# Kernel tuning notes

Hardware: AMD Instinct MI355X
Metric: run time of the kernel (lower is better)

Reference implementation:

```python
import jax, jax.numpy as jnp
import numpy as np

N = 100000   # number of nodes
E = 400000   # number of edges
C = 16       # n_in_channels == n_out_channels
L = 16       # node_conv2 .. node_conv17
EPS = 1e-5   # BatchNorm eps


def _bn(h, g, b):
    # training-mode BatchNorm1d over the edge/batch axis (biased variance)
    mu = h.mean(0)
    var = h.var(0)
    return (h - mu) * jax.lax.rsqrt(var + EPS) * g + b


def setup_inputs() -> dict:
    key = jax.random.key(0)
    ks = jax.random.split(key, 6)
    return {
        "edge_features": jax.random.normal(ks[0], (E, C), jnp.float32),
        "edge_index": jax.random.randint(ks[1], (2, E), 0, N),
        "angles": jax.random.normal(ks[2], (E,), jnp.float32),
        "Wn": jax.random.normal(ks[3], (L, C, 2 * C), jnp.float32) / np.sqrt(2.0 * C),
        "bn": jnp.zeros((L, C), jnp.float32),
        "gn": jnp.ones((L, C), jnp.float32),
        "btn": jnp.zeros((L, C), jnp.float32),
        "We": jax.random.normal(ks[4], (C, 2 * C), jnp.float32) / np.sqrt(2.0 * C),
        "be": jnp.zeros((C,), jnp.float32),
        "ge": jnp.ones((C,), jnp.float32),
        "bte": jnp.zeros((C,), jnp.float32),
    }


def _forward(edge_features, edge_index, Wn, bn, gn, btn, We, be, ge, bte):
    src, dst = edge_index[0], edge_index[1]

    # EdgeConvNoNodes: init node features = mean of incident edge features (both endpoints)
    idx = jnp.concatenate([src, dst])                       # [2E]
    feats = jnp.concatenate([edge_features, edge_features], axis=0)
    deg = jax.ops.segment_sum(jnp.ones((2 * E,), edge_features.dtype), idx, N)
    x = jax.ops.segment_sum(feats, idx, N) / jnp.clip(deg, 1.0)[:, None]  # [N, C]

    # in-degree for mean aggregation of the 16 NodeConv1 layers
    deg_in = jnp.clip(jax.ops.segment_sum(jnp.ones((E,), x.dtype), dst, N), 1.0)[:, None]

    def step(x, p):
        W, b, g, bt = p
        # message: Linear(cat(x_i, x_j)) -> BN -> LeakyReLU on [E, C]
        m = jnp.concatenate([x[dst], x[src]], axis=1) @ W.T + b
        m = jax.nn.leaky_relu(_bn(m, g, bt))
        # mean aggregation at target nodes
        return jax.ops.segment_sum(m, dst, N) / deg_in, None

    x, _ = jax.lax.scan(step, x, (Wn, bn, gn, btn))

    # EdgeConv2: per-edge MLP on both edge directions, BN stats shared over [2E]
    pair = jnp.concatenate(
        [jnp.concatenate([x[src], x[dst]], axis=1),
         jnp.concatenate([x[dst], x[src]], axis=1)], axis=0)  # [2E, 2C]
    e = jax.nn.leaky_relu(_bn(pair @ We.T + be, ge, bte))      # [2E, C]
    e_fwd, e_bwd = e[:E], e[E:]
    edge_out = 0.5 * (e_fwd + e_bwd)                           # symmetric edge feature
    side_loss = jnp.mean((e_fwd - e_bwd) ** 2)                 # symmetry side loss
    return edge_out, side_loss


def reference(edge_features, edge_index, angles, Wn, bn, gn, btn, We, be, ge, bte):
    # `angles` is accepted but unused, matching the original forward
    return _forward(edge_features, edge_index, Wn, bn, gn, btn, We, be, ge, bte)
```

## Files before the change

### kernel.cpp

```cpp
#include <hip/hip_runtime.h>
#include <hip/hip_fp16.h>
#include <cstdint>
#include <cstddef>

#define NN 100000
#define EE 400000
#define CC 16
#define LL 16
#define NB 16

typedef unsigned int uint;

__device__ __forceinline__ float lrelu(float v){ return v > 0.0f ? v : 0.01f*v; }

__device__ __forceinline__ float waveSum(float v){
#pragma unroll
  for (int off = 32; off >= 1; off >>= 1) v += __shfl_xor(v, off);
  return v;
}

__device__ __forceinline__ uint pack_h2(float a, float b){
  __half2 h = __floats2half2_rn(a, b);
  return *reinterpret_cast<uint*>(&h);
}
__device__ __forceinline__ float2 unpack_h2(uint v){
  __half2 h = *reinterpret_cast<__half2*>(&v);
  return __half22float2(h);
}

__device__ __forceinline__ void unpack_row(const uint* __restrict__ xh, int n, float* f){
  const uint4* p = (const uint4*)(xh + (size_t)n*8);
  uint4 r0 = p[0], r1 = p[1];
  uint w[8] = {r0.x,r0.y,r0.z,r0.w, r1.x,r1.y,r1.z,r1.w};
#pragma unroll
  for (int q=0;q<8;q++){ float2 v = unpack_h2(w[q]); f[2*q]=v.x; f[2*q+1]=v.y; }
}

__global__ __launch_bounds__(256) void k_count(const int* __restrict__ ei,
    int* __restrict__ cdst, int* __restrict__ csrc)
{
  int t = blockIdx.x*256 + threadIdx.x;
  if (t >= EE) return;
  int s = ei[t], d = ei[EE + t];
  atomicAdd(&cdst[d], 1);
  atomicAdd(&csrc[s], 1);
}

__device__ __forceinline__ void scan_one(const int* __restrict__ cnt,
    int* __restrict__ rp, int* __restrict__ bsums, int n, int* sd)
{
  int tid = threadIdx.x;
  int base = blockIdx.x*1024 + tid*4;
  int v0=0,v1=0,v2=0,v3=0;
  if (base+0 < n) v0 = cnt[base+0];
  if (base+1 < n) v1 = cnt[base+1];
  if (base+2 < n) v2 = cnt[base+2];
  if (base+3 < n) v3 = cnt[base+3];
  int tot = v0+v1+v2+v3;
  sd[tid] = tot; __syncthreads();
  for (int off=1; off<256; off<<=1){
    int add = (tid>=off) ? sd[tid-off] : 0;
    __syncthreads();
    sd[tid] += add;
    __syncthreads();
  }
  int excl = sd[tid] - tot;
  if (base+0 < n) rp[base+0] = excl;
  if (base+1 < n) rp[base+1] = excl+v0;
  if (base+2 < n) rp[base+2] = excl+v0+v1;
  if (base+3 < n) rp[base+3] = excl+v0+v1+v2;
  if (tid==255) bsums[blockIdx.x] = sd[255];
  __syncthreads();
}

__global__ __launch_bounds__(256) void k_scan1(const int* __restrict__ ca,
    int* __restrict__ rpa, int* __restrict__ bsa,
    const int* __restrict__ cb, int* __restrict__ rpb, int* __restrict__ bsb, int n)
{
  __shared__ int sd[256];
  scan_one(ca, rpa, bsa, n, sd);
  scan_one(cb, rpb, bsb, n, sd);
}

__device__ __forceinline__ void scan2_one(const int* __restrict__ bsums,
    int* __restrict__ boff, int nseg, int* sd)
{
  int tid = threadIdx.x;
  int v = (tid < nseg) ? bsums[tid] : 0;
  sd[tid] = v; __syncthreads();
  for (int off=1; off<256; off<<=1){
    int add = (tid>=off) ? sd[tid-off] : 0;
    __syncthreads();
    sd[tid] += add;
    __syncthreads();
  }
  if (tid < nseg) boff[tid] = sd[tid] - v;
  __syncthreads();
}

__global__ __launch_bounds__(256) void k_scan2(const int* __restrict__ bsa,
    int* __restrict__ boffa, const int* __restrict__ bsb, int* __restrict__ boffb, int nseg)
{
  __shared__ int sd[256];
  scan2_one(bsa, boffa, nseg, sd);
  scan2_one(bsb, boffb, nseg, sd);
}

__global__ __launch_bounds__(256) void k_scan3(
    int* __restrict__ rpa, int* __restrict__ cura, const int* __restrict__ boffa, int totala,
    int* __restrict__ rpb, int* __restrict__ curb, const int* __restrict__ boffb, int totalb, int n)
{
  int adda = boffa[blockIdx.x];
  int addb = boffb[blockIdx.x];
  int base = blockIdx.x*1024 + threadIdx.x*4;
#pragma unroll
  for (int i=0;i<4;i++){
    if (base+i < n){
      int va = rpa[base+i] + adda; rpa[base+i] = va; cura[base+i] = va;
      int vb = rpb[base+i] + addb; rpb[base+i] = vb; curb[base+i] = vb;
    }
  }
  if (blockIdx.x==0 && threadIdx.x==0){ rpa[n] = totala; rpb[n] = totalb; }
}

__global__ __launch_bounds__(256) void k_fill(const int* __restrict__ ei,
    int* __restrict__ cur, int4* __restrict__ sd4,
    int* __restrict__ curs, int* __restrict__ lsrc)
{
  int t = blockIdx.x*256 + threadIdx.x;
  if (t >= EE) return;
  int s = ei[t], d = ei[EE + t];
  int p = atomicAdd(&cur[d], 1);
  sd4[p] = make_int4(s, d, t, 0);
  int ps = atomicAdd(&curs[s], 1);
  lsrc[ps] = t;
}

__global__ __launch_bounds__(256) void k_gather0(const float* __restrict__ ef,
    const int4* __restrict__ sd4, const int* __restrict__ rp,
    const int* __restrict__ lsrc, const int* __restrict__ rps,
    uint* __restrict__ xh, float* __restrict__ invdeg)
{
  int t = blockIdx.x*256 + threadIdx.x;
  if (t >= NN*8) return;
  int n = t >> 3, cp = t & 7;
  int bd = rp[n], ed = rp[n+1];
  int bs = rps[n], es = rps[n+1];
  float a0 = 0.0f, a1 = 0.0f;
  for (int i=bd; i<ed; i++){
    const float2* p = (const float2*)(ef + (size_t)sd4[i].z*CC + 2*cp);
    float2 v = *p;
    a0 += v.x; a1 += v.y;
  }
  for (int i=bs; i<es; i++){
    const float2* p = (const float2*)(ef + (size_t)lsrc[i]*CC + 2*cp);
    float2 v = *p;
    a0 += v.x; a1 += v.y;
  }
  float dg = fmaxf((float)((ed-bd)+(es-bs)), 1.0f);
  xh[(size_t)n*8 + cp] = pack_h2(a0/dg, a1/dg);
  if (cp == 0){
    invdeg[n] = 1.0f / fmaxf((float)(ed-bd), 1.0f);
  }
}

__global__ __launch_bounds__(256) void k_edge(const uint* __restrict__ xh,
    const int4* __restrict__ sd4,
    const float* __restrict__ W, const float* __restrict__ b,
    uint* __restrict__ mh, double* __restrict__ st)
{
  __shared__ float sW[512];
  __shared__ float sb16[16];
  __shared__ float sredS[64], sredQ[64];
  for (int i=threadIdx.x; i<512; i+=256) sW[i] = W[i];
  if (threadIdx.x < 16) sb16[threadIdx.x] = b[threadIdx.x];
  __syncthreads();

  int t = blockIdx.x*256 + threadIdx.x;
  int e0 = 2*t, e1 = 2*t+1;
  bool val = (e1 < EE);
  float acc0[16], acc1[16];
  if (val){
    int4 p0 = sd4[e0], p1 = sd4[e1];
    float xa[32], xb[32];
    unpack_row(xh, p0.y, xa);
    unpack_row(xh, p0.x, xa + 16);
    unpack_row(xh, p1.y, xb);
    unpack_row(xh, p1.x, xb + 16);
#pragma unroll
    for (int c=0;c<16;c++){
      const float* wr = sW + c*32;
      float a0 = sb16[c], a1 = sb16[c];
#pragma unroll
      for (int k=0;k<32;k++){
        float w = wr[k];
        a0 = fmaf(w, xa[k], a0);
        a1 = fmaf(w, xb[k], a1);
      }
      acc0[c]=a0; acc1[c]=a1;
    }
    uint w0[8], w1[8];
#pragma unroll
    for (int q=0;q<8;q++){
      w0[q] = pack_h2(acc0[2*q], acc0[2*q+1]);
      w1[q] = pack_h2(acc1[2*q], acc1[2*q+1]);
    }
    uint4* po0 = (uint4*)(mh + (size_t)e0*8);
    po0[0] = make_uint4(w0[0],w0[1],w0[2],w0[3]);
    po0[1] = make_uint4(w0[4],w0[5],w0[6],w0[7]);
    uint4* po1 = (uint4*)(mh + (size_t)e1*8);
    po1[0] = make_uint4(w1[0],w1[1],w1[2],w1[3]);
    po1[1] = make_uint4(w1[4],w1[5],w1[6],w1[7]);
  } else {
#pragma unroll
    for (int c=0;c<16;c++){ acc0[c]=0.0f; acc1[c]=0.0f; }
  }

  int lane = threadIdx.x & 63, w = threadIdx.x >> 6;
#pragma unroll
  for (int c=0;c<16;c++){
    float rs = acc0[c] + acc1[c];
    float rq = acc0[c]*acc0[c] + acc1[c]*acc1[c];
    rs = waveSum(rs); rq = waveSum(rq);
    if (lane == 0){ sredS[w*16+c] = rs; sredQ[w*16+c] = rq; }
  }
  __syncthreads();
  double* stb = st + (size_t)(blockIdx.x & (NB-1))*32;
  if (threadIdx.x < 16){
    int c = threadIdx.x;
    float tot = sredS[c] + sredS[16+c] + sredS[32+c] + sredS[48+c];
    unsafeAtomicAdd(&stb[c], (double)tot);
  } else if (threadIdx.x < 32){
    int c = threadIdx.x - 16;
    float tot = sredQ[c] + sredQ[16+c] + sredQ[32+c] + sredQ[48+c];
    unsafeAtomicAdd(&stb[16+c], (double)tot);
  }
}

__global__ __launch_bounds__(256) void k_node(const uint* __restrict__ mh,
    const int* __restrict__ rp,
    const float* __restrict__ invdeg, const double* __restrict__ st,
    const float* __restrict__ g, const float* __restrict__ bt,
    uint* __restrict__ xhout)
{
  __shared__ float sA[16], sB[16];
  if (threadIdx.x < 16){
    int c = threadIdx.x;
    double S = 0.0, Q = 0.0;
#pragma unroll
    for (int k=0;k<NB;k++){ S += st[k*32 + c]; Q += st[k*32 + 16 + c]; }
    double mu  = S * (1.0/EE);
    double var = Q * (1.0/EE) - mu*mu;
    float sc = rsqrtf((float)var + 1e-5f);
    float A = sc * g[c];
    sA[c] = A; sB[c] = bt[c] - (float)mu * A;
  }
  __syncthreads();
  int t = blockIdx.x*256 + threadIdx.x;
  int n = t >> 3, cp = t & 7;
  if (n >= NN) return;
  float A0 = sA[2*cp], B0 = sB[2*cp];
  float A1 = sA[2*cp+1], B1 = sB[2*cp+1];
  int beg = rp[n], end = rp[n+1];
  float a0 = 0.0f, a1 = 0.0f;
  for (int i=beg; i<end; i++){
    float2 v = unpack_h2(mh[(size_t)i*8 + cp]);
    a0 += lrelu(fmaf(A0, v.x, B0));
    a1 += lrelu(fmaf(A1, v.y, B1));
  }
  float iv = invdeg[n];
  xhout[(size_t)n*8 + cp] = pack_h2(a0*iv, a1*iv);
}

__global__ __launch_bounds__(256) void k_uvf(const uint* __restrict__ xh,
    const float* __restrict__ W, const float* __restrict__ b,
    uint* __restrict__ u, uint* __restrict__ v)
{
  __shared__ float sW[512];
  __shared__ float sb16[16];
  for (int i=threadIdx.x; i<512; i+=256) sW[i] = W[i];
  if (threadIdx.x < 16) sb16[threadIdx.x] = b[threadIdx.x];
  __syncthreads();
  int n = blockIdx.x*256 + threadIdx.x;
  if (n >= NN) return;
  float xr[16];
  unpack_row(xh, n, xr);
  uint up[8], vp[8];
#pragma unroll
  for (int q=0;q<8;q++){
    int c0 = 2*q, c1 = 2*q+1;
    const float* w0 = sW + c0*32;
    const float* w1 = sW + c1*32;
    float u0 = sb16[c0], u1 = sb16[c1], v0 = 0.f, v1 = 0.f;
#pragma unroll
    for (int k=0;k<16;k++){
      float xv = xr[k];
      u0 = fmaf(w0[k],    xv, u0);
      v0 = fmaf(w0[16+k], xv, v0);
      u1 = fmaf(w1[k],    xv, u1);
      v1 = fmaf(w1[16+k], xv, v1);
    }
    up[q] = pack_h2(u0,u1);
    vp[q] = pack_h2(v0,v1);
  }
  uint4* pu = (uint4*)(u + (size_t)n*8);
  pu[0] = make_uint4(up[0],up[1],up[2],up[3]);
  pu[1] = make_uint4(up[4],up[5],up[6],up[7]);
  uint4* pv = (uint4*)(v + (size_t)n*8);
  pv[0] = make_uint4(vp[0],vp[1],vp[2],vp[3]);
  pv[1] = make_uint4(vp[4],vp[5],vp[6],vp[7]);
}

__global__ __launch_bounds__(256) void k_final1(
    const uint* __restrict__ uf, const uint* __restrict__ vf,
    const int* __restrict__ ei, double* __restrict__ st)
{
  __shared__ float sredS[64], sredQ[64];
  int t = blockIdx.x*256 + threadIdx.x;
  float ls[16], lq[16];
#pragma unroll
  for (int c=0;c<16;c++){ ls[c]=0.f; lq[c]=0.f; }
  if (t < EE){
    int s = ei[t], d = ei[EE+t];
    const uint4* pus = (const uint4*)(uf + (size_t)s*8);
    const uint4* pvd = (const uint4*)(vf + (size_t)d*8);
    const uint4* pud = (const uint4*)(uf + (size_t)d*8);
    const uint4* pvs = (const uint4*)(vf + (size_t)s*8);
    uint4 us0=pus[0], us1=pus[1], vd0=pvd[0], vd1=pvd[1];
    uint4 ud0=pud[0], ud1=pud[1], vs0=pvs[0], vs1=pvs[1];
    uint usw[8]={us0.x,us0.y,us0.z,us0.w, us1.x,us1.y,us1.z,us1.w};
    uint vdw[8]={vd0.x,vd0.y,vd0.z,vd0.w, vd1.x,vd1.y,vd1.z,vd1.w};
    uint udw[8]={ud0.x,ud0.y,ud0.z,ud0.w, ud1.x,ud1.y,ud1.z,ud1.w};
    uint vsw[8]={vs0.x,vs0.y,vs0.z,vs0.w, vs1.x,vs1.y,vs1.z,vs1.w};
#pragma unroll
    for (int q=0;q<8;q++){
      float2 a = unpack_h2(usw[q]), bq = unpack_h2(vdw[q]);
      float2 cc = unpack_h2(udw[q]), dd = unpack_h2(vsw[q]);
      float f0 = a.x + bq.x, f1 = a.y + bq.y;
      float g0 = cc.x + dd.x, g1 = cc.y + dd.y;
      ls[2*q]   += f0 + g0; lq[2*q]   += f0*f0 + g0*g0;
      ls[2*q+1] += f1 + g1; lq[2*q+1] += f1*f1 + g1*g1;
    }
  }
  int lane = threadIdx.x & 63, w = threadIdx.x >> 6;
#pragma unroll
  for (int c=0;c<16;c++){
    float rs = waveSum(ls[c]);
    float rq = waveSum(lq[c]);
    if (lane == 0){ sredS[w*16+c] = rs; sredQ[w*16+c] = rq; }
  }
  __syncthreads();
  double* stb = st + (size_t)(blockIdx.x & (NB-1))*32;
  if (threadIdx.x < 16){
    int c = threadIdx.x;
    float tot = sredS[c] + sredS[16+c] + sredS[32+c] + sredS[48+c];
    unsafeAtomicAdd(&stb[c], (double)tot);
  } else if (threadIdx.x < 32){
    int c = threadIdx.x - 16;
    float tot = sredQ[c] + sredQ[16+c] + sredQ[32+c] + sredQ[48+c];
    unsafeAtomicAdd(&stb[16+c], (double)tot);
  }
}

__global__ __launch_bounds__(256) void k_final2(
    const uint* __restrict__ uf, const uint* __restrict__ vf,
    const int* __restrict__ ei, const double* __restrict__ st,
    const float* __restrict__ g, const float* __restrict__ bt,
    float* __restrict__ out, double* __restrict__ loss)
{
  __shared__ float sA[16], sB[16];
  __shared__ float sl[4];
  if (threadIdx.x < 16){
    int c = threadIdx.x;
    double S = 0.0, Q = 0.0;
#pragma unroll
    for (int k=0;k<NB;k++){ S += st[k*32 + c]; Q += st[k*32 + 16 + c]; }
    double mu  = S * (1.0/(2.0*EE));
    double var = Q * (1.0/(2.0*EE)) - mu*mu;
    float sc = rsqrtf((float)var + 1e-5f);
    float A = sc * g[c];
    sA[c] = A; sB[c] = bt[c] - (float)mu * A;
  }
  __syncthreads();

  int t = blockIdx.x*256 + threadIdx.x;
  float lsum = 0.0f;
  if (t < EE){
    int s = ei[t], d = ei[EE+t];
    const uint4* pus = (const uint4*)(uf + (size_t)s*8);
    const uint4* pvd = (const uint4*)(vf + (size_t)d*8);
    const uint4* pud = (const uint4*)(uf + (size_t)d*8);
    const uint4* pvs = (const uint4*)(vf + (size_t)s*8);
    uint4 us0=pus[0], us1=pus[1], vd0=pvd[0], vd1=pvd[1];
    uint4 ud0=pud[0], ud1=pud[1], vs0=pvs[0], vs1=pvs[1];
    uint usw[8]={us0.x,us0.y,us0.z,us0.w, us1.x,us1.y,us1.z,us1.w};
    uint vdw[8]={vd0.x,vd0.y,vd0.z,vd0.w, vd1.x,vd1.y,vd1.z,vd1.w};
    uint udw[8]={ud0.x,ud0.y,ud0.z,ud0.w, ud1.x,ud1.y,ud1.z,ud1.w};
    uint vsw[8]={vs0.x,vs0.y,vs0.z,vs0.w, vs1.x,vs1.y,vs1.z,vs1.w};
    float fo[16];
#pragma unroll
    for (int q=0;q<8;q++){
      float2 a = unpack_h2(usw[q]), bq = unpack_h2(vdw[q]);
      float2 cc = unpack_h2(udw[q]), dd = unpack_h2(vsw[q]);
      int c0 = 2*q, c1 = 2*q+1;
      float e0 = lrelu(fmaf(sA[c0], a.x + bq.x, sB[c0]));
      float b0 = lrelu(fmaf(sA[c0], cc.x + dd.x, sB[c0]));
      float e1 = lrelu(fmaf(sA[c1], a.y + bq.y, sB[c1]));
      float b1 = lrelu(fmaf(sA[c1], cc.y + dd.y, sB[c1]));
      fo[c0] = 0.5f*(e0 + b0);
      fo[c1] = 0.5f*(e1 + b1);
      float d0 = e0 - b0, d1 = e1 - b1;
      lsum = fmaf(d0, d0, lsum);
      lsum = fmaf(d1, d1, lsum);
    }
    float4* po = (float4*)(out + (size_t)t*CC);
    po[0]=make_float4(fo[0],fo[1],fo[2],fo[3]);
    po[1]=make_float4(fo[4],fo[5],fo[6],fo[7]);
    po[2]=make_float4(fo[8],fo[9],fo[10],fo[11]);
    po[3]=make_float4(fo[12],fo[13],fo[14],fo[15]);
  }
  lsum = waveSum(lsum);
  int lane = threadIdx.x & 63, w = threadIdx.x >> 6;
  if (lane == 0) sl[w] = lsum;
  __syncthreads();
  if (threadIdx.x == 0)
    unsafeAtomicAdd(&loss[blockIdx.x & (NB-1)], (double)(sl[0]+sl[1]+sl[2]+sl[3]));
}

__global__ void k_final3(float* __restrict__ out, const double* __restrict__ loss)
{
  double s = 0.0;
#pragma unroll
  for (int k=0;k<NB;k++) s += loss[k];
  out[(size_t)EE*CC] = (float)(s * (1.0/((double)EE*CC)));
}

extern "C" void kernel_launch(void* const* d_in, const int* in_sizes, int n_in,
                              void* d_out, int out_size, void* d_ws, size_t ws_size,
                              hipStream_t stream)
{
  (void)in_sizes; (void)n_in; (void)out_size; (void)ws_size;
  const float* ef  = (const float*)d_in[0];
  const int*   ei  = (const int*)d_in[1];
  const float* Wn  = (const float*)d_in[3];
  const float* bn  = (const float*)d_in[4];
  const float* gn  = (const float*)d_in[5];
  const float* btn = (const float*)d_in[6];
  const float* We  = (const float*)d_in[7];
  const float* be  = (const float*)d_in[8];
  const float* ge  = (const float*)d_in[9];
  const float* bte = (const float*)d_in[10];
  float* out = (float*)d_out;
  char* ws = (char*)d_ws;

  size_t off = 0;
  auto alloc = [&](size_t bytes)->size_t{
    size_t r = off; off = (off + bytes + 255) & ~(size_t)255; return r;
  };
  size_t o_xha    = alloc((size_t)NN*8*4);
  size_t o_xhb    = alloc((size_t)NN*8*4);
  size_t o_mh     = alloc((size_t)EE*8*4);
  size_t o_uf     = alloc((size_t)NN*8*4);
  size_t o_vf     = alloc((size_t)NN*8*4);
  size_t o_cdst   = alloc((size_t)NN*4);
  size_t o_csrc   = alloc((size_t)NN*4);
  size_t o_rp     = alloc((size_t)(NN+1)*4);
  size_t o_rps    = alloc((size_t)(NN+1)*4);
  size_t o_cur    = alloc((size_t)NN*4);
  size_t o_curs   = alloc((size_t)NN*4);
  size_t o_sd4    = alloc((size_t)EE*16);
  size_t o_lsrc   = alloc((size_t)EE*4);
  size_t o_bsum   = alloc(512);
  size_t o_bsum2  = alloc(512);
  size_t o_boff   = alloc(512);
  size_t o_boff2  = alloc(512);
  size_t o_stats  = alloc((size_t)(17*NB*32 + NB)*8);
  size_t o_invdeg = alloc((size_t)NN*4);

  uint*   xh_a    = (uint*)(ws + o_xha);
  uint*   xh_b    = (uint*)(ws + o_xhb);
  uint*   m_h     = (uint*)(ws + o_mh);
  uint*   u_f     = (uint*)(ws + o_uf);
  uint*   v_f     = (uint*)(ws + o_vf);
  int*    cdst    = (int*)(ws + o_cdst);
  int*    csrc    = (int*)(ws + o_csrc);
  int*    rp      = (int*)(ws + o_rp);
  int*    rps     = (int*)(ws + o_rps);
  int*    cur     = (int*)(ws + o_cur);
  int*    curs    = (int*)(ws + o_curs);
  int4*   sd4     = (int4*)(ws + o_sd4);
  int*    lsrc    = (int*)(ws + o_lsrc);
  int*    bsum    = (int*)(ws + o_bsum);
  int*    bsum2   = (int*)(ws + o_bsum2);
  int*    boff    = (int*)(ws + o_boff);
  int*    boff2   = (int*)(ws + o_boff2);
  double* stats   = (double*)(ws + o_stats);
  double* lossd   = stats + (size_t)17*NB*32;
  float*  invdeg  = (float*)(ws + o_invdeg);

  const int GB_E  = (EE + 255)/256;
  const int GB_E2 = (EE/2 + 255)/256;
  const int GB_N8 = (NN*8 + 255)/256;
  const int GB_N  = (NN + 255)/256;
  const int NSEG  = (NN + 1023)/1024;

  hipMemsetAsync(cdst, 0, (size_t)NN*4, stream);
  hipMemsetAsync(csrc, 0, (size_t)NN*4, stream);
  hipMemsetAsync(stats, 0, (size_t)(17*NB*32 + NB)*8, stream);

  k_count<<<GB_E, 256, 0, stream>>>(ei, cdst, csrc);
  k_scan1<<<NSEG, 256, 0, stream>>>(cdst, rp, bsum, csrc, rps, bsum2, NN);
  k_scan2<<<1, 256, 0, stream>>>(bsum, boff, bsum2, boff2, NSEG);
  k_scan3<<<NSEG, 256, 0, stream>>>(rp, cur, boff, EE, rps, curs, boff2, EE, NN);
  k_fill<<<GB_E, 256, 0, stream>>>(ei, cur, sd4, curs, lsrc);
  k_gather0<<<GB_N8, 256, 0, stream>>>(ef, sd4, rp, lsrc, rps, xh_a, invdeg);

  uint* xc = xh_a;
  uint* xn = xh_b;
  for (int l = 0; l < LL; ++l){
    double* st = stats + (size_t)l*NB*32;
    const float* Wl = Wn + (size_t)l*CC*2*CC;
    const float* bl = bn + (size_t)l*CC;
    k_edge<<<GB_E2, 256, 0, stream>>>(xc, sd4, Wl, bl, m_h, st);
    k_node<<<GB_N8, 256, 0, stream>>>(m_h, rp, invdeg, st,
                                      gn + (size_t)l*CC, btn + (size_t)l*CC, xn);
    uint* tmp = xc; xc = xn; xn = tmp;
  }

  double* stF = stats + (size_t)LL*NB*32;
  k_uvf<<<GB_N, 256, 0, stream>>>(xc, We, be, u_f, v_f);
  k_final1<<<GB_E, 256, 0, stream>>>(u_f, v_f, ei, stF);
  k_final2<<<GB_E, 256, 0, stream>>>(u_f, v_f, ei, stF, ge, bte, out, lossd);
  k_final3<<<1, 1, 0, stream>>>(out, lossd);
}
```

Measured before the change: 775.6 us.

## Split edge index into int2 pairs, shrink edge blocks, fuse final projection into last node pass

The CSR edge record changes from int4 (src,dst,eid,pad) to an int2 src/dst array plus a separate edge-id array, halving the bytes k_edge reads per edge in each of the 16 layers. k_edge now runs 128-thread blocks, which doubles the block count and the number of stats atomics. The last layer's node aggregation is templated to compute the u/v projection through shared memory directly, removing the k_uvf launch and one round trip of x through global memory. The two count memsets are merged into one, and the node grid drops its bounds check because NN*8 divides evenly by 256.

```diff
diff --git a/kernel.cpp b/kernel.cpp
--- a/kernel.cpp
+++ b/kernel.cpp
@@ -124,20 +124,21 @@
 }
 
 __global__ __launch_bounds__(256) void k_fill(const int* __restrict__ ei,
-    int* __restrict__ cur, int4* __restrict__ sd4,
+    int* __restrict__ cur, int2* __restrict__ sdp, int* __restrict__ eidp,
     int* __restrict__ curs, int* __restrict__ lsrc)
 {
   int t = blockIdx.x*256 + threadIdx.x;
   if (t >= EE) return;
   int s = ei[t], d = ei[EE + t];
   int p = atomicAdd(&cur[d], 1);
-  sd4[p] = make_int4(s, d, t, 0);
+  sdp[p] = make_int2(s, d);
+  eidp[p] = t;
   int ps = atomicAdd(&curs[s], 1);
   lsrc[ps] = t;
 }
 
 __global__ __launch_bounds__(256) void k_gather0(const float* __restrict__ ef,
-    const int4* __restrict__ sd4, const int* __restrict__ rp,
+    const int* __restrict__ eidp, const int* __restrict__ rp,
     const int* __restrict__ lsrc, const int* __restrict__ rps,
     uint* __restrict__ xh, float* __restrict__ invdeg)
 {
@@ -148,7 +149,7 @@
   int bs = rps[n], es = rps[n+1];
   float a0 = 0.0f, a1 = 0.0f;
   for (int i=bd; i<ed; i++){
-    const float2* p = (const float2*)(ef + (size_t)sd4[i].z*CC + 2*cp);
+    const float2* p = (const float2*)(ef + (size_t)eidp[i]*CC + 2*cp);
     float2 v = *p;
     a0 += v.x; a1 += v.y;
   }
@@ -164,24 +165,24 @@
   }
 }
 
-__global__ __launch_bounds__(256) void k_edge(const uint* __restrict__ xh,
-    const int4* __restrict__ sd4,
+__global__ __launch_bounds__(128) void k_edge(const uint* __restrict__ xh,
+    const int2* __restrict__ sdp,
     const float* __restrict__ W, const float* __restrict__ b,
     uint* __restrict__ mh, double* __restrict__ st)
 {
   __shared__ float sW[512];
   __shared__ float sb16[16];
-  __shared__ float sredS[64], sredQ[64];
-  for (int i=threadIdx.x; i<512; i+=256) sW[i] = W[i];
+  __shared__ float sredS[32], sredQ[32];
+  for (int i=threadIdx.x; i<512; i+=128) sW[i] = W[i];
   if (threadIdx.x < 16) sb16[threadIdx.x] = b[threadIdx.x];
   __syncthreads();
 
-  int t = blockIdx.x*256 + threadIdx.x;
+  int t = blockIdx.x*128 + threadIdx.x;
   int e0 = 2*t, e1 = 2*t+1;
   bool val = (e1 < EE);
   float acc0[16], acc1[16];
   if (val){
-    int4 p0 = sd4[e0], p1 = sd4[e1];
+    int2 p0 = sdp[e0], p1 = sdp[e1];
     float xa[32], xb[32];
     unpack_row(xh, p0.y, xa);
     unpack_row(xh, p0.x, xa + 16);
@@ -228,24 +229,34 @@
   double* stb = st + (size_t)(blockIdx.x & (NB-1))*32;
   if (threadIdx.x < 16){
     int c = threadIdx.x;
-    float tot = sredS[c] + sredS[16+c] + sredS[32+c] + sredS[48+c];
+    float tot = sredS[c] + sredS[16+c];
     unsafeAtomicAdd(&stb[c], (double)tot);
   } else if (threadIdx.x < 32){
     int c = threadIdx.x - 16;
-    float tot = sredQ[c] + sredQ[16+c] + sredQ[32+c] + sredQ[48+c];
+    float tot = sredQ[c] + sredQ[16+c];
     unsafeAtomicAdd(&stb[16+c], (double)tot);
   }
 }
 
+template<bool LAST>
 __global__ __launch_bounds__(256) void k_node(const uint* __restrict__ mh,
     const int* __restrict__ rp,
     const float* __restrict__ invdeg, const double* __restrict__ st,
     const float* __restrict__ g, const float* __restrict__ bt,
-    uint* __restrict__ xhout)
+    const float* __restrict__ We, const float* __restrict__ be,
+    uint* __restrict__ xhout, uint* __restrict__ uf, uint* __restrict__ vf)
 {
   __shared__ float sA[16], sB[16];
-  if (threadIdx.x < 16){
-    int c = threadIdx.x;
+  __shared__ float sW[512];
+  __shared__ float sbn[16];
+  __shared__ float sX[32][17];
+  const int tid = threadIdx.x;
+  if (LAST){
+    for (int i=tid;i<512;i+=256) sW[i] = We[i];
+    if (tid < 16) sbn[tid] = be[tid];
+  }
+  if (tid < 16){
+    int c = tid;
     double S = 0.0, Q = 0.0;
 #pragma unroll
     for (int k=0;k<NB;k++){ S += st[k*32 + c]; Q += st[k*32 + 16 + c]; }
@@ -256,9 +267,8 @@
     sA[c] = A; sB[c] = bt[c] - (float)mu * A;
   }
   __syncthreads();
-  int t = blockIdx.x*256 + threadIdx.x;
-  int n = t >> 3, cp = t & 7;
-  if (n >= NN) return;
+  int t = blockIdx.x*256 + tid;
+  int n = t >> 3, cp = t & 7, nl = tid >> 3;
   float A0 = sA[2*cp], B0 = sB[2*cp];
   float A1 = sA[2*cp+1], B1 = sB[2*cp+1];
   int beg = rp[n], end = rp[n+1];
@@ -269,29 +279,18 @@
     a1 += lrelu(fmaf(A1, v.y, B1));
   }
   float iv = invdeg[n];
-  xhout[(size_t)n*8 + cp] = pack_h2(a0*iv, a1*iv);
-}
-
-__global__ __launch_bounds__(256) void k_uvf(const uint* __restrict__ xh,
-    const float* __restrict__ W, const float* __restrict__ b,
-    uint* __restrict__ u, uint* __restrict__ v)
-{
-  __shared__ float sW[512];
-  __shared__ float sb16[16];
-  for (int i=threadIdx.x; i<512; i+=256) sW[i] = W[i];
-  if (threadIdx.x < 16) sb16[threadIdx.x] = b[threadIdx.x];
-  __syncthreads();
-  int n = blockIdx.x*256 + threadIdx.x;
-  if (n >= NN) return;
-  float xr[16];
-  unpack_row(xh, n, xr);
-  uint up[8], vp[8];
-#pragma unroll
-  for (int q=0;q<8;q++){
-    int c0 = 2*q, c1 = 2*q+1;
+  float xv0 = a0*iv, xv1 = a1*iv;
+
+  if (!LAST){
+    xhout[(size_t)n*8 + cp] = pack_h2(xv0, xv1);
+  } else {
+    sX[nl][2*cp] = xv0; sX[nl][2*cp+1] = xv1;
+    __syncthreads();
+    int c0 = 2*cp, c1 = 2*cp+1;
     const float* w0 = sW + c0*32;
     const float* w1 = sW + c1*32;
-    float u0 = sb16[c0], u1 = sb16[c1], v0 = 0.f, v1 = 0.f;
+    const float* xr = sX[nl];
+    float u0 = sbn[c0], u1 = sbn[c1], v0 = 0.f, v1 = 0.f;
 #pragma unroll
     for (int k=0;k<16;k++){
       float xv = xr[k];
@@ -300,15 +299,9 @@
       u1 = fmaf(w1[k],    xv, u1);
       v1 = fmaf(w1[16+k], xv, v1);
     }
-    up[q] = pack_h2(u0,u1);
-    vp[q] = pack_h2(v0,v1);
-  }
-  uint4* pu = (uint4*)(u + (size_t)n*8);
-  pu[0] = make_uint4(up[0],up[1],up[2],up[3]);
-  pu[1] = make_uint4(up[4],up[5],up[6],up[7]);
-  uint4* pv = (uint4*)(v + (size_t)n*8);
-  pv[0] = make_uint4(vp[0],vp[1],vp[2],vp[3]);
-  pv[1] = make_uint4(vp[4],vp[5],vp[6],vp[7]);
+    uf[(size_t)n*8 + cp] = pack_h2(u0, u1);
+    vf[(size_t)n*8 + cp] = pack_h2(v0, v1);
+  }
 }
 
 __global__ __launch_bounds__(256) void k_final1(
@@ -457,6 +450,7 @@
   auto alloc = [&](size_t bytes)->size_t{
     size_t r = off; off = (off + bytes + 255) & ~(size_t)255; return r;
   };
+  const size_t SZN = ((size_t)NN*4 + 255) & ~(size_t)255;
   size_t o_xha    = alloc((size_t)NN*8*4);
   size_t o_xhb    = alloc((size_t)NN*8*4);
   size_t o_mh     = alloc((size_t)EE*8*4);
@@ -468,7 +462,8 @@
   size_t o_rps    = alloc((size_t)(NN+1)*4);
   size_t o_cur    = alloc((size_t)NN*4);
   size_t o_curs   = alloc((size_t)NN*4);
-  size_t o_sd4    = alloc((size_t)EE*16);
+  size_t o_sdp    = alloc((size_t)EE*8);
+  size_t o_eidp   = alloc((size_t)EE*4);
   size_t o_lsrc   = alloc((size_t)EE*4);
   size_t o_bsum   = alloc(512);
   size_t o_bsum2  = alloc(512);
@@ -488,7 +483,8 @@
   int*    rps     = (int*)(ws + o_rps);
   int*    cur     = (int*)(ws + o_cur);
   int*    curs    = (int*)(ws + o_curs);
-  int4*   sd4     = (int4*)(ws + o_sd4);
+  int2*   sdp     = (int2*)(ws + o_sdp);
+  int*    eidp    = (int*)(ws + o_eidp);
   int*    lsrc    = (int*)(ws + o_lsrc);
   int*    bsum    = (int*)(ws + o_bsum);
   int*    bsum2   = (int*)(ws + o_bsum2);
@@ -499,21 +495,19 @@
   float*  invdeg  = (float*)(ws + o_invdeg);
 
   const int GB_E  = (EE + 255)/256;
-  const int GB_E2 = (EE/2 + 255)/256;
-  const int GB_N8 = (NN*8 + 255)/256;
-  const int GB_N  = (NN + 255)/256;
+  const int GB_E2 = (EE/2 + 127)/128;
+  const int GB_N8 = (NN*8)/256;
   const int NSEG  = (NN + 1023)/1024;
 
-  hipMemsetAsync(cdst, 0, (size_t)NN*4, stream);
-  hipMemsetAsync(csrc, 0, (size_t)NN*4, stream);
+  hipMemsetAsync(cdst, 0, 2*SZN, stream);
   hipMemsetAsync(stats, 0, (size_t)(17*NB*32 + NB)*8, stream);
 
   k_count<<<GB_E, 256, 0, stream>>>(ei, cdst, csrc);
   k_scan1<<<NSEG, 256, 0, stream>>>(cdst, rp, bsum, csrc, rps, bsum2, NN);
   k_scan2<<<1, 256, 0, stream>>>(bsum, boff, bsum2, boff2, NSEG);
   k_scan3<<<NSEG, 256, 0, stream>>>(rp, cur, boff, EE, rps, curs, boff2, EE, NN);
-  k_fill<<<GB_E, 256, 0, stream>>>(ei, cur, sd4, curs, lsrc);
-  k_gather0<<<GB_N8, 256, 0, stream>>>(ef, sd4, rp, lsrc, rps, xh_a, invdeg);
+  k_fill<<<GB_E, 256, 0, stream>>>(ei, cur, sdp, eidp, curs, lsrc);
+  k_gather0<<<GB_N8, 256, 0, stream>>>(ef, eidp, rp, lsrc, rps, xh_a, invdeg);
 
   uint* xc = xh_a;
   uint* xn = xh_b;
@@ -521,14 +515,20 @@
     double* st = stats + (size_t)l*NB*32;
     const float* Wl = Wn + (size_t)l*CC*2*CC;
     const float* bl = bn + (size_t)l*CC;
-    k_edge<<<GB_E2, 256, 0, stream>>>(xc, sd4, Wl, bl, m_h, st);
-    k_node<<<GB_N8, 256, 0, stream>>>(m_h, rp, invdeg, st,
-                                      gn + (size_t)l*CC, btn + (size_t)l*CC, xn);
-    uint* tmp = xc; xc = xn; xn = tmp;
+    k_edge<<<GB_E2, 128, 0, stream>>>(xc, sdp, Wl, bl, m_h, st);
+    if (l < LL-1){
+      k_node<false><<<GB_N8, 256, 0, stream>>>(m_h, rp, invdeg, st,
+          gn + (size_t)l*CC, btn + (size_t)l*CC, nullptr, nullptr,
+          xn, nullptr, nullptr);
+      uint* tmp = xc; xc = xn; xn = tmp;
+    } else {
+      k_node<true><<<GB_N8, 256, 0, stream>>>(m_h, rp, invdeg, st,
+          gn + (size_t)l*CC, btn + (size_t)l*CC, We, be,
+          nullptr, u_f, v_f);
+    }
   }
 
   double* stF = stats + (size_t)LL*NB*32;
-  k_uvf<<<GB_N, 256, 0, stream>>>(xc, We, be, u_f, v_f);
   k_final1<<<GB_E, 256, 0, stream>>>(u_f, v_f, ei, stF);
   k_final2<<<GB_E, 256, 0, stream>>>(u_f, v_f, ei, stF, ge, bte, out, lossd);
   k_final3<<<1, 1, 0, stream>>>(out, lossd);
```

Result: no change. 764.7 us (median of 2 runs) (-1.4%).
